# Kernel tuning notes

Hardware: AMD Instinct MI355X
Metric: run time of the kernel (lower is better)

## Reference

```python
import jax, jax.numpy as jnp
import numpy as np

EMB = 1024
HID = 1024
VOCAB = 50257
MAX_LEN = 4096


def _xavier(key, shape):
    fan_in, fan_out = shape[1], shape[0]
    lim = jnp.sqrt(6.0 / (fan_in + fan_out)).astype(jnp.float32)
    return jax.random.uniform(key, shape, jnp.float32, -lim, lim)


def setup_inputs() -> dict:
    key = jax.random.key(0)
    ks = jax.random.split(key, 10)
    return {
        "attn_vec": jax.random.normal(ks[0], (MAX_LEN, 1, HID), jnp.float32),
        "input": jax.random.normal(ks[1], (EMB,), jnp.float32),
        "hidden": jax.random.normal(ks[2], (1, 1, HID), jnp.float32),
        "cell": jax.random.normal(ks[3], (1, 1, HID), jnp.float32),
        "W_ih": _xavier(ks[4], (4 * HID, EMB)),
        "W_hh": _xavier(ks[5], (4 * HID, HID)),
        "b_ih": jnp.zeros((4 * HID,), jnp.float32),
        "b_hh": jnp.zeros((4 * HID,), jnp.float32),
        "fc1_w": _xavier(ks[6], (HID, 2 * HID)),
        "fc1_b": jnp.zeros((HID,), jnp.float32),
        "fc2_w": _xavier(ks[7], (VOCAB, HID)),
        "fc2_b": jnp.zeros((VOCAB,), jnp.float32),
    }


def reference(attn_vec, input, hidden, cell, W_ih, W_hh, b_ih, b_hh, fc1_w, fc1_b, fc2_w, fc2_b):
    x = input.reshape(-1)          # [E]
    h = hidden.reshape(-1)         # [H]
    c = cell.reshape(-1)           # [H]
    # single-step LSTM (PyTorch gate order: i, f, g, o)
    gates = W_ih @ x + b_ih + W_hh @ h + b_hh       # [4H]
    i_g, f_g, g_g, o_g = jnp.split(gates, 4)
    i_g = jax.nn.sigmoid(i_g)
    f_g = jax.nn.sigmoid(f_g)
    g_g = jnp.tanh(g_g)
    o_g = jax.nn.sigmoid(o_g)
    c_new = f_g * c + i_g * g_g
    h_new = o_g * jnp.tanh(c_new)                   # [H]
    # dot-product attention over encoder states (vectorized, replacing the python loop)
    a = attn_vec[:, 0, :]                           # [L, H]
    scores = a @ h_new                              # [L]
    w = jax.nn.softmax(scores, axis=0)              # [L]
    ctx = a.T @ w                                   # [H]
    # concat + 2-layer MLP (no nonlinearity between fc1 and fc2) + log-softmax
    concat = jnp.concatenate([ctx, h_new], axis=0)  # [2H]
    out = fc2_w @ (fc1_w @ concat + fc1_b) + fc2_b  # [V]
    logp = jax.nn.log_softmax(out, axis=0)
    return (logp, (h_new.reshape(1, 1, -1), c_new.reshape(1, 1, -1)))
```

## Files before the change

### kernel.cpp

```cpp
#include <hip/hip_runtime.h>
#include <math.h>

#define HID   1024
#define VOCAB 50257
#define SEQ   4096

__device__ __forceinline__ float wave_sum(float v) {
    #pragma unroll
    for (int o = 32; o > 0; o >>= 1) v += __shfl_xor(v, o, 64);
    return v;
}
__device__ __forceinline__ float wave_max(float v) {
    #pragma unroll
    for (int o = 32; o > 0; o >>= 1) v = fmaxf(v, __shfl_xor(v, o, 64));
    return v;
}
__device__ __forceinline__ float sigmoidf(float x) {
    return 1.0f / (1.0f + expf(-x));
}
__device__ __forceinline__ int enc_f(float f) {
    int k = __float_as_int(f);
    return k >= 0 ? k : k ^ 0x7FFFFFFF;
}
__device__ __forceinline__ float dec_f(int k) {
    return __int_as_float(k >= 0 ? k : k ^ 0x7FFFFFFF);
}

__global__ __launch_bounds__(256) void k_gates_lstm(
        const float* __restrict__ W_ih, const float* __restrict__ W_hh,
        const float* __restrict__ x, const float* __restrict__ h,
        const float* __restrict__ b_ih, const float* __restrict__ b_hh,
        const float* __restrict__ c_old,
        float* __restrict__ hnew, float* __restrict__ ctx,
        float* __restrict__ out_h, float* __restrict__ out_c,
        int* __restrict__ gmax, float* __restrict__ Ssum,
        int* __restrict__ lmax) {
    __shared__ float g4[4];
    int t = blockIdx.x;
    int wave = threadIdx.x >> 6, lane = threadIdx.x & 63;
    int row = wave * HID + t;
    const float4* wi = (const float4*)(W_ih + (size_t)row * HID);
    const float4* wh = (const float4*)(W_hh + (size_t)row * HID);
    const float4* xv = (const float4*)x;
    const float4* hv = (const float4*)h;
    float s = 0.f;
    #pragma unroll
    for (int i = 0; i < 4; ++i) {
        int idx = lane + 64 * i;
        float4 a = wi[idx], b = xv[idx];
        s += a.x * b.x + a.y * b.y + a.z * b.z + a.w * b.w;
        float4 c = wh[idx], d = hv[idx];
        s += c.x * d.x + c.y * d.y + c.z * d.z + c.w * d.w;
    }
    s = wave_sum(s);
    if (lane == 0) g4[wave] = s + b_ih[row] + b_hh[row];
    __syncthreads();
    if (threadIdx.x == 0) {
        float ig = sigmoidf(g4[0]);
        float fg = sigmoidf(g4[1]);
        float gg = tanhf(g4[2]);
        float og = sigmoidf(g4[3]);
        float cn = fg * c_old[t] + ig * gg;
        float hn = og * tanhf(cn);
        hnew[t] = hn; out_h[t] = hn; out_c[t] = cn;
        ctx[t] = 0.f;
        if (t == 0) {
            *gmax = (int)0x80000000;
            *lmax = (int)0x80000000;
            *Ssum = 0.f;
        }
    }
}

__global__ __launch_bounds__(256) void k_scores(
        const float* __restrict__ a, const float* __restrict__ h,
        float* __restrict__ scores, int* __restrict__ gmax) {
    __shared__ float bm[4];
    int wave = threadIdx.x >> 6, lane = threadIdx.x & 63;
    int row = blockIdx.x * 4 + wave;
    const float4* av = (const float4*)(a + (size_t)row * HID);
    const float4* hv = (const float4*)h;
    float s = 0.f;
    #pragma unroll
    for (int i = 0; i < 4; ++i) {
        int idx = lane + 64 * i;
        float4 p = av[idx], q = hv[idx];
        s += p.x * q.x + p.y * q.y + p.z * q.z + p.w * q.w;
    }
    s = wave_sum(s);
    if (lane == 0) { scores[row] = s; bm[wave] = s; }
    __syncthreads();
    if (threadIdx.x == 0) {
        float m = fmaxf(fmaxf(bm[0], bm[1]), fmaxf(bm[2], bm[3]));
        atomicMax(gmax, enc_f(m));
    }
}

__global__ __launch_bounds__(256) void k_ctx(
        const float* __restrict__ a, const float* __restrict__ scores,
        const int* __restrict__ gmax, float* __restrict__ ctx,
        float* __restrict__ Ssum) {
    __shared__ float e[64];
    int tid = threadIdx.x;
    int col = blockIdx.x * 256 + tid;
    int s0 = blockIdx.y * 64;
    float m = dec_f(*gmax);
    if (tid < 64) {
        float ev = expf(scores[s0 + tid] - m);
        e[tid] = ev;
        float ssum = wave_sum(ev);
        if (tid == 0 && blockIdx.x == 0) atomicAdd(Ssum, ssum);
    }
    __syncthreads();
    float acc = 0.f;
    #pragma unroll 8
    for (int j = 0; j < 64; ++j)
        acc += e[j] * a[(size_t)(s0 + j) * HID + col];
    atomicAdd(&ctx[col], acc);
}

__global__ __launch_bounds__(256) void k_fc1(
        const float* __restrict__ W, const float* __restrict__ ctx,
        const float* __restrict__ h, const float* __restrict__ b,
        const float* __restrict__ Ssum, float* __restrict__ out) {
    int wave = threadIdx.x >> 6, lane = threadIdx.x & 63;
    int row = blockIdx.x * 4 + wave;
    const float4* wr = (const float4*)(W + (size_t)row * 2 * HID);
    const float4* cv = (const float4*)ctx;
    const float4* hv = (const float4*)h;
    float sc = 0.f, sh = 0.f;
    #pragma unroll
    for (int i = 0; i < 4; ++i) {
        int idx = lane + 64 * i;
        float4 p = wr[idx], q = cv[idx];
        sc += p.x * q.x + p.y * q.y + p.z * q.z + p.w * q.w;
        float4 r = wr[256 + idx], t = hv[idx];
        sh += r.x * t.x + r.y * t.y + r.z * t.z + r.w * t.w;
    }
    sc = wave_sum(sc);
    sh = wave_sum(sh);
    if (lane == 0) out[row] = sc / (*Ssum) + sh + b[row];
}

__global__ __launch_bounds__(256) void k_fc2(
        const float* __restrict__ W, const float* __restrict__ v,
        const float* __restrict__ b, float* __restrict__ out,
        int* __restrict__ lmax) {
    __shared__ float bm[4];
    int wave = threadIdx.x >> 6, lane = threadIdx.x & 63;
    int row = blockIdx.x * 4 + wave;
    int valid = row < VOCAB;
    int rv = valid ? row : (VOCAB - 1);
    const float4* wr = (const float4*)(W + (size_t)rv * HID);
    const float4* vv = (const float4*)v;
    float s = 0.f;
    #pragma unroll
    for (int i = 0; i < 4; ++i) {
        int idx = lane + 64 * i;
        float4 p = wr[idx], q = vv[idx];
        s += p.x * q.x + p.y * q.y + p.z * q.z + p.w * q.w;
    }
    s = wave_sum(s);
    if (lane == 0) {
        float val = s + b[rv];
        if (valid) out[row] = val;
        bm[wave] = valid ? val : -INFINITY;
    }
    __syncthreads();
    if (threadIdx.x == 0) {
        float m = fmaxf(fmaxf(bm[0], bm[1]), fmaxf(bm[2], bm[3]));
        atomicMax(lmax, enc_f(m));
    }
}

__global__ __launch_bounds__(1024) void k_lse(
        const float* __restrict__ logits, const int* __restrict__ lmax,
        float* __restrict__ red_out) {
    __shared__ float red[16];
    int tid = threadIdx.x, wave = tid >> 6, lane = tid & 63;
    float m = dec_f(*lmax);
    const float4* lv = (const float4*)logits;
    const int N4 = VOCAB / 4;
    float s = (tid == 0) ? expf(logits[VOCAB - 1] - m) : 0.f;
    for (int i = tid; i < N4; i += 1024) {
        float4 v = lv[i];
        s += expf(v.x - m) + expf(v.y - m) + expf(v.z - m) + expf(v.w - m);
    }
    s = wave_sum(s);
    if (lane == 0) red[wave] = s;
    __syncthreads();
    if (tid < 64) {
        float ss = (tid < 16) ? red[tid] : 0.f;
        ss = wave_sum(ss);
        if (tid == 0) { red_out[0] = m; red_out[1] = logf(ss); }
    }
}

__global__ __launch_bounds__(256) void k_final(
        const float* __restrict__ logits, const float* __restrict__ red,
        float* __restrict__ out) {
    const int N4 = VOCAB / 4;
    int i = blockIdx.x * 256 + threadIdx.x;
    float c = red[0] + red[1];
    if (i < N4) {
        float4 v = ((const float4*)logits)[i];
        v.x -= c; v.y -= c; v.z -= c; v.w -= c;
        ((float4*)out)[i] = v;
    } else if (i == N4) {
        out[VOCAB - 1] = logits[VOCAB - 1] - c;
    }
}

extern "C" void kernel_launch(void* const* d_in, const int* in_sizes, int n_in,
                              void* d_out, int out_size, void* d_ws, size_t ws_size,
                              hipStream_t stream) {
    const float* attn  = (const float*)d_in[0];
    const float* x     = (const float*)d_in[1];
    const float* h     = (const float*)d_in[2];
    const float* c     = (const float*)d_in[3];
    const float* W_ih  = (const float*)d_in[4];
    const float* W_hh  = (const float*)d_in[5];
    const float* b_ih  = (const float*)d_in[6];
    const float* b_hh  = (const float*)d_in[7];
    const float* fc1_w = (const float*)d_in[8];
    const float* fc1_b = (const float*)d_in[9];
    const float* fc2_w = (const float*)d_in[10];
    const float* fc2_b = (const float*)d_in[11];

    float* out = (float*)d_out;
    float* ws  = (float*)d_ws;
    float* hnew   = ws;
    float* scores = ws + 1024;
    float* ctx    = ws + 5120;
    float* fc1o   = ws + 6144;
    float* logits = ws + 7168;
    float* red    = ws + 57440;
    int*   gmax   = (int*)(ws + 57456);
    float* Ssum   = ws + 57457;
    int*   lmax   = (int*)(ws + 57458);

    k_gates_lstm<<<1024, 256, 0, stream>>>(W_ih, W_hh, x, h, b_ih, b_hh, c,
                                           hnew, ctx, out + VOCAB,
                                           out + VOCAB + HID, gmax, Ssum, lmax);
    k_scores    <<<1024, 256, 0, stream>>>(attn, hnew, scores, gmax);
    k_ctx       <<<dim3(4, 64), 256, 0, stream>>>(attn, scores, gmax, ctx, Ssum);
    k_fc1       <<<256, 256, 0, stream>>>(fc1_w, ctx, hnew, fc1_b, Ssum, fc1o);
    k_fc2       <<<(VOCAB + 3) / 4, 256, 0, stream>>>(fc2_w, fc1o, fc2_b,
                                                      logits, lmax);
    k_lse       <<<1, 1024, 0, stream>>>(logits, lmax, red);
    k_final     <<<(VOCAB / 4 + 256) / 256, 256, 0, stream>>>(logits, red, out);
}
```

Before: 448.8 us.

## Replace atomics with dedicated softmax, two-pass ctx reduction and split LSE

Removes the global atomicMax and atomicAdd reductions (score max, ctx accumulation, logit max, sum) in favour of deterministic kernels. The attention softmax now runs in its own single-block kernel, ctx is built from partial sums written to a buffer and reduced in a second kernel, and the log-sum-exp runs across 13 blocks before a tiny merge kernel. This cuts atomic contention and replaces the single-block LSE pass with a multi-block one, at the cost of three extra kernel launches.

Result: faster. 369.5 us (-17.7%).

```diff
diff --git a/kernel.cpp b/kernel.cpp
--- a/kernel.cpp
+++ b/kernel.cpp
@@ -4,6 +4,7 @@
 #define HID   1024
 #define VOCAB 50257
 #define SEQ   4096
+#define NLSE  13
 
 __device__ __forceinline__ float wave_sum(float v) {
     #pragma unroll
@@ -17,13 +18,6 @@
 }
 __device__ __forceinline__ float sigmoidf(float x) {
     return 1.0f / (1.0f + expf(-x));
-}
-__device__ __forceinline__ int enc_f(float f) {
-    int k = __float_as_int(f);
-    return k >= 0 ? k : k ^ 0x7FFFFFFF;
-}
-__device__ __forceinline__ float dec_f(int k) {
-    return __int_as_float(k >= 0 ? k : k ^ 0x7FFFFFFF);
 }
 
 __global__ __launch_bounds__(256) void k_gates_lstm(
@@ -31,10 +25,8 @@
         const float* __restrict__ x, const float* __restrict__ h,
         const float* __restrict__ b_ih, const float* __restrict__ b_hh,
         const float* __restrict__ c_old,
-        float* __restrict__ hnew, float* __restrict__ ctx,
-        float* __restrict__ out_h, float* __restrict__ out_c,
-        int* __restrict__ gmax, float* __restrict__ Ssum,
-        int* __restrict__ lmax) {
+        float* __restrict__ hnew,
+        float* __restrict__ out_h, float* __restrict__ out_c) {
     __shared__ float g4[4];
     int t = blockIdx.x;
     int wave = threadIdx.x >> 6, lane = threadIdx.x & 63;
@@ -63,19 +55,12 @@
         float cn = fg * c_old[t] + ig * gg;
         float hn = og * tanhf(cn);
         hnew[t] = hn; out_h[t] = hn; out_c[t] = cn;
-        ctx[t] = 0.f;
-        if (t == 0) {
-            *gmax = (int)0x80000000;
-            *lmax = (int)0x80000000;
-            *Ssum = 0.f;
-        }
     }
 }
 
 __global__ __launch_bounds__(256) void k_scores(
         const float* __restrict__ a, const float* __restrict__ h,
-        float* __restrict__ scores, int* __restrict__ gmax) {
-    __shared__ float bm[4];
+        float* __restrict__ scores) {
     int wave = threadIdx.x >> 6, lane = threadIdx.x & 63;
     int row = blockIdx.x * 4 + wave;
     const float4* av = (const float4*)(a + (size_t)row * HID);
@@ -88,70 +73,97 @@
         s += p.x * q.x + p.y * q.y + p.z * q.z + p.w * q.w;
     }
     s = wave_sum(s);
-    if (lane == 0) { scores[row] = s; bm[wave] = s; }
-    __syncthreads();
-    if (threadIdx.x == 0) {
-        float m = fmaxf(fmaxf(bm[0], bm[1]), fmaxf(bm[2], bm[3]));
-        atomicMax(gmax, enc_f(m));
-    }
-}
-
-__global__ __launch_bounds__(256) void k_ctx(
-        const float* __restrict__ a, const float* __restrict__ scores,
-        const int* __restrict__ gmax, float* __restrict__ ctx,
-        float* __restrict__ Ssum) {
+    if (lane == 0) scores[row] = s;
+}
+
+__global__ __launch_bounds__(1024) void k_softmax(float* __restrict__ scores) {
+    __shared__ float red[32];
+    int tid = threadIdx.x, wave = tid >> 6, lane = tid & 63;
+    float4 v = ((const float4*)scores)[tid];
+    float m = fmaxf(fmaxf(v.x, v.y), fmaxf(v.z, v.w));
+    m = wave_max(m);
+    if (lane == 0) red[wave] = m;
+    __syncthreads();
+    if (tid < 64) {
+        float mm = (tid < 16) ? red[tid] : -INFINITY;
+        mm = wave_max(mm);
+        if (tid == 0) red[0] = mm;
+    }
+    __syncthreads();
+    m = red[0];
+    float4 e;
+    e.x = expf(v.x - m); e.y = expf(v.y - m);
+    e.z = expf(v.z - m); e.w = expf(v.w - m);
+    float s = e.x + e.y + e.z + e.w;
+    s = wave_sum(s);
+    if (lane == 0) red[16 + wave] = s;
+    __syncthreads();
+    if (tid < 64) {
+        float ss = (tid < 16) ? red[16 + tid] : 0.f;
+        ss = wave_sum(ss);
+        if (tid == 0) red[16] = ss;
+    }
+    __syncthreads();
+    float inv = 1.0f / red[16];
+    e.x *= inv; e.y *= inv; e.z *= inv; e.w *= inv;
+    ((float4*)scores)[tid] = e;
+}
+
+__global__ __launch_bounds__(256) void k_ctx_part(
+        const float* __restrict__ a, const float* __restrict__ w,
+        float* __restrict__ part) {
     __shared__ float e[64];
     int tid = threadIdx.x;
     int col = blockIdx.x * 256 + tid;
     int s0 = blockIdx.y * 64;
-    float m = dec_f(*gmax);
-    if (tid < 64) {
-        float ev = expf(scores[s0 + tid] - m);
-        e[tid] = ev;
-        float ssum = wave_sum(ev);
-        if (tid == 0 && blockIdx.x == 0) atomicAdd(Ssum, ssum);
-    }
+    if (tid < 64) e[tid] = w[s0 + tid];
     __syncthreads();
     float acc = 0.f;
     #pragma unroll 8
     for (int j = 0; j < 64; ++j)
         acc += e[j] * a[(size_t)(s0 + j) * HID + col];
-    atomicAdd(&ctx[col], acc);
+    part[blockIdx.y * HID + col] = acc;
+}
+
+__global__ __launch_bounds__(256) void k_ctx_red(
+        const float* __restrict__ part, float* __restrict__ ctx) {
+    int col = blockIdx.x * 256 + threadIdx.x;
+    float acc = 0.f;
+    #pragma unroll
+    for (int j = 0; j < 64; ++j)
+        acc += part[j * HID + col];
+    ctx[col] = acc;
 }
 
 __global__ __launch_bounds__(256) void k_fc1(
         const float* __restrict__ W, const float* __restrict__ ctx,
         const float* __restrict__ h, const float* __restrict__ b,
-        const float* __restrict__ Ssum, float* __restrict__ out) {
+        float* __restrict__ out) {
     int wave = threadIdx.x >> 6, lane = threadIdx.x & 63;
     int row = blockIdx.x * 4 + wave;
     const float4* wr = (const float4*)(W + (size_t)row * 2 * HID);
     const float4* cv = (const float4*)ctx;
     const float4* hv = (const float4*)h;
-    float sc = 0.f, sh = 0.f;
+    float s = 0.f;
     #pragma unroll
     for (int i = 0; i < 4; ++i) {
         int idx = lane + 64 * i;
         float4 p = wr[idx], q = cv[idx];
-        sc += p.x * q.x + p.y * q.y + p.z * q.z + p.w * q.w;
+        s += p.x * q.x + p.y * q.y + p.z * q.z + p.w * q.w;
         float4 r = wr[256 + idx], t = hv[idx];
-        sh += r.x * t.x + r.y * t.y + r.z * t.z + r.w * t.w;
-    }
-    sc = wave_sum(sc);
-    sh = wave_sum(sh);
-    if (lane == 0) out[row] = sc / (*Ssum) + sh + b[row];
+        s += r.x * t.x + r.y * t.y + r.z * t.z + r.w * t.w;
+    }
+    s = wave_sum(s);
+    if (lane == 0) out[row] = s + b[row];
 }
 
 __global__ __launch_bounds__(256) void k_fc2(
         const float* __restrict__ W, const float* __restrict__ v,
-        const float* __restrict__ b, float* __restrict__ out,
-        int* __restrict__ lmax) {
-    __shared__ float bm[4];
+        const float* __restrict__ b, float* __restrict__ out) {
     int wave = threadIdx.x >> 6, lane = threadIdx.x & 63;
     int row = blockIdx.x * 4 + wave;
-    int valid = row < VOCAB;
-    int rv = valid ? row : (VOCAB - 1);
-    const float4* wr = (const float4*)(W + (size_t)rv * HID);
+    if (row >= VOCAB) return;
+    const float4* wr = (const float4*)(W + (size_t)row * HID);
     const float4* vv = (const float4*)v;
     float s = 0.f;
     #pragma unroll
@@ -161,39 +173,58 @@
         s += p.x * q.x + p.y * q.y + p.z * q.z + p.w * q.w;
     }
     s = wave_sum(s);
-    if (lane == 0) {
-        float val = s + b[rv];
-        if (valid) out[row] = val;
-        bm[wave] = valid ? val : -INFINITY;
-    }
-    __syncthreads();
-    if (threadIdx.x == 0) {
-        float m = fmaxf(fmaxf(bm[0], bm[1]), fmaxf(bm[2], bm[3]));
-        atomicMax(lmax, enc_f(m));
-    }
-}
-
-__global__ __launch_bounds__(1024) void k_lse(
-        const float* __restrict__ logits, const int* __restrict__ lmax,
-        float* __restrict__ red_out) {
-    __shared__ float red[16];
+    if (lane == 0) out[row] = s + b[row];
+}
+
+__global__ __launch_bounds__(1024) void k_lse1(
+        const float* __restrict__ logits,
+        float* __restrict__ pm, float* __restrict__ ps) {
+    __shared__ float red[17];
     int tid = threadIdx.x, wave = tid >> 6, lane = tid & 63;
-    float m = dec_f(*lmax);
-    const float4* lv = (const float4*)logits;
-    const int N4 = VOCAB / 4;
-    float s = (tid == 0) ? expf(logits[VOCAB - 1] - m) : 0.f;
-    for (int i = tid; i < N4; i += 1024) {
-        float4 v = lv[i];
-        s += expf(v.x - m) + expf(v.y - m) + expf(v.z - m) + expf(v.w - m);
-    }
-    s = wave_sum(s);
+    int i4 = blockIdx.x * 1024 + tid;
+    int i0 = i4 * 4;
+    float x0 = -INFINITY, x1 = -INFINITY, x2 = -INFINITY, x3 = -INFINITY;
+    if (i0 + 3 < VOCAB) {
+        float4 v = ((const float4*)logits)[i4];
+        x0 = v.x; x1 = v.y; x2 = v.z; x3 = v.w;
+    } else {
+        if (i0     < VOCAB) x0 = logits[i0];
+        if (i0 + 1 < VOCAB) x1 = logits[i0 + 1];
+        if (i0 + 2 < VOCAB) x2 = logits[i0 + 2];
+        if (i0 + 3 < VOCAB) x3 = logits[i0 + 3];
+    }
+    float m = fmaxf(fmaxf(x0, x1), fmaxf(x2, x3));
+    m = wave_max(m);
+    if (lane == 0) red[wave] = m;
+    __syncthreads();
+    if (tid < 64) {
+        float mm = (tid < 16) ? red[tid] : -INFINITY;
+        mm = wave_max(mm);
+        if (tid == 0) red[16] = mm;
+    }
+    __syncthreads();
+    m = red[16];
+    float s = expf(x0 - m) + expf(x1 - m) + expf(x2 - m) + expf(x3 - m);
+    s = wave_sum(s);
+    __syncthreads();
     if (lane == 0) red[wave] = s;
     __syncthreads();
     if (tid < 64) {
         float ss = (tid < 16) ? red[tid] : 0.f;
         ss = wave_sum(ss);
-        if (tid == 0) { red_out[0] = m; red_out[1] = logf(ss); }
-    }
+        if (tid == 0) { pm[blockIdx.x] = m; ps[blockIdx.x] = ss; }
+    }
+}
+
+__global__ __launch_bounds__(64) void k_lse2(
+        const float* __restrict__ pm, const float* __restrict__ ps,
+        float* __restrict__ red_out) {
+    int lane = threadIdx.x;
+    float m = (lane < NLSE) ? pm[lane] : -INFINITY;
+    float M = wave_max(m);
+    float s = (lane < NLSE) ? ps[lane] * expf(pm[lane] - M) : 0.f;
+    float S = wave_sum(s);
+    if (lane == 0) { red_out[0] = M; red_out[1] = logf(S); }
 }
 
 __global__ __launch_bounds__(256) void k_final(
@@ -233,20 +264,23 @@
     float* scores = ws + 1024;
     float* ctx    = ws + 5120;
     float* fc1o   = ws + 6144;
-    float* logits = ws + 7168;
-    float* red    = ws + 57440;
-    int*   gmax   = (int*)(ws + 57456);
-    float* Ssum   = ws + 57457;
-    int*   lmax   = (int*)(ws + 57458);
+    float* buf    = ws + 7168;
+    float* pm     = ws + 72704;
+    float* ps     = ws + 72720;
+    float* red    = ws + 72736;
+
+    float* part   = buf;
+    float* logits = buf;
 
     k_gates_lstm<<<1024, 256, 0, stream>>>(W_ih, W_hh, x, h, b_ih, b_hh, c,
-                                           hnew, ctx, out + VOCAB,
-                                           out + VOCAB + HID, gmax, Ssum, lmax);
-    k_scores    <<<1024, 256, 0, stream>>>(attn, hnew, scores, gmax);
-    k_ctx       <<<dim3(4, 64), 256, 0, stream>>>(attn, scores, gmax, ctx, Ssum);
-    k_fc1       <<<256, 256, 0, stream>>>(fc1_w, ctx, hnew, fc1_b, Ssum, fc1o);
-    k_fc2       <<<(VOCAB + 3) / 4, 256, 0, stream>>>(fc2_w, fc1o, fc2_b,
-                                                      logits, lmax);
-    k_lse       <<<1, 1024, 0, stream>>>(logits, lmax, red);
+                                           hnew, out + VOCAB, out + VOCAB + HID);
+    k_scores    <<<1024, 256, 0, stream>>>(attn, hnew, scores);
+    k_softmax   <<<1, 1024, 0, stream>>>(scores);
+    k_ctx_part  <<<dim3(4, 64), 256, 0, stream>>>(attn, scores, part);
+    k_ctx_red   <<<4, 256, 0, stream>>>(part, ctx);
+    k_fc1       <<<256, 256, 0, stream>>>(fc1_w, ctx, hnew, fc1_b, fc1o);
+    k_fc2       <<<(VOCAB + 3) / 4, 256, 0, stream>>>(fc2_w, fc1o, fc2_b, logits);
+    k_lse1      <<<NLSE, 1024, 0, stream>>>(logits, pm, ps);
+    k_lse2      <<<1, 64, 0, stream>>>(pm, ps, red);
     k_final     <<<(VOCAB / 4 + 256) / 256, 256, 0, stream>>>(logits, red, out);
 }
```
